# Performance work log

Hardware: AMD Instinct MI355X
Metric: run time of the kernel (lower is better)

## Reference

```python
import jax, jax.numpy as jnp
import numpy as np

OS = 14            # output_size
GRID = 2           # ceil(roi_size/OS) = ceil(28/14) = 2 (boxes are built 28x28, sampling_ratio=-1)
NODES = OS * OS    # 196 graph nodes
EPS = 1e-5         # BatchNorm eps
K, B, C, H, W = 256, 4, 256, 112, 112


def _bn_relu(x, g, b, m, v):
    # eval-mode BatchNorm2d followed by ReLU (bn_act_conv prefix)
    s = jax.lax.rsqrt(v + EPS)
    xn = (x - m[None, :, None, None]) * s[None, :, None, None]
    return jax.nn.relu(xn * g[None, :, None, None] + b[None, :, None, None])


def _conv(x, w, b, pad):
    y = jax.lax.conv_general_dilated(x, w, (1, 1), [(pad, pad), (pad, pad)],
                                     dimension_numbers=('NCHW', 'OIHW', 'NCHW'))
    return y + b[None, :, None, None]


def _roi_align(sem, boxes):
    # torchvision roi_align, spatial_scale=1.0, aligned=False, sampling_ratio=-1 (static grid=2)
    Bs, Cc, Hh, Ww = sem.shape
    bidx = boxes[:, 0].astype(jnp.int32)
    x1, y1, x2, y2 = boxes[:, 1], boxes[:, 2], boxes[:, 3], boxes[:, 4]
    bw = jnp.maximum(x2 - x1, 1.0) / OS
    bh = jnp.maximum(y2 - y1, 1.0) / OS
    t = (jnp.arange(OS * GRID, dtype=sem.dtype) + 0.5) / GRID   # pw*GRID+ix collapsed
    xs = x1[:, None] + bw[:, None] * t                          # [K, 28]
    ys = y1[:, None] + bh[:, None] * t

    def prep(c, L):
        m = (c >= -1.0) & (c <= L)
        cc = jnp.clip(c, 0.0, L - 1)
        lo = jnp.floor(cc).astype(jnp.int32)
        hi = jnp.minimum(lo + 1, L - 1)
        return m, lo, hi, cc - lo

    my, yl, yh, ly = prep(ys, Hh)
    mx, xl, xh, lx = prep(xs, Ww)
    semt = jnp.transpose(sem, (0, 2, 3, 1))  # [B,H,W,C]

    def gat(ya, xa):
        return semt[bidx[:, None, None], ya[:, :, None], xa[:, None, :]]  # [K,28,28,C]

    ly_ = ly[:, :, None, None]
    lx_ = lx[:, None, :, None]
    val = (gat(yl, xl) * (1 - ly_) * (1 - lx_) + gat(yl, xh) * (1 - ly_) * lx_
           + gat(yh, xl) * ly_ * (1 - lx_) + gat(yh, xh) * ly_ * lx_)
    val = jnp.where((my[:, :, None] & mx[:, None, :])[..., None], val, 0.0)
    val = val.reshape(-1, OS, GRID, OS, GRID, Cc).mean(axis=(2, 4))  # avg over sampling grid
    return jnp.transpose(val, (0, 3, 1, 2))  # [K,C,14,14]


def _gcn_agg(A, x):
    # PyG gcn_norm on a fully-connected weighted graph (self loops already present):
    # deg[j] = sum_i A[i,j] (scatter on col); out[j] = sum_i d^-1/2[i] A[i,j] d^-1/2[j] x[i]
    deg = A.sum(axis=1)                 # [K,196]
    dis = jax.lax.rsqrt(deg)            # sigmoid weights > 0 => no zero degree
    Nrm = dis[:, :, None] * A * dis[:, None, :]
    return jnp.einsum('kij,kif->kjf', Nrm, x)


def _forward(roi_feature, semantic, boxes,
             bn_sem_g, bn_sem_b, bn_sem_m, bn_sem_v, conv_sem_w, conv_sem_b,
             bn_fpn_g, bn_fpn_b, bn_fpn_m, bn_fpn_v, conv_fpn_w, conv_fpn_b,
             bn_aff_g, bn_aff_b, bn_aff_m, bn_aff_v, conv_aff_w, conv_aff_b,
             gcn1_w, gcn1_b, gcn2_w, gcn2_b):
    roi_sem = _roi_align(semantic, boxes)                                   # [K,256,14,14]
    a = (_conv(_bn_relu(roi_sem, bn_sem_g, bn_sem_b, bn_sem_m, bn_sem_v), conv_sem_w, conv_sem_b, 1)
         + _conv(_bn_relu(roi_feature, bn_fpn_g, bn_fpn_b, bn_fpn_m, bn_fpn_v), conv_fpn_w, conv_fpn_b, 1))
    aff = _conv(_bn_relu(a, bn_aff_g, bn_aff_b, bn_aff_m, bn_aff_v), conv_aff_w, conv_aff_b, 0)
    A = jax.nn.sigmoid(aff.reshape(-1, NODES, NODES))                       # [K,196,196]
    X = roi_feature.reshape(-1, C, NODES).transpose(0, 2, 1)                # [K,196,256] node feats
    x1 = jax.nn.relu(_gcn_agg(A, X @ gcn1_w) + gcn1_b)                      # GCNConv(256,16)+ReLU
    x2 = _gcn_agg(A, x1 @ gcn2_w) + gcn2_b                                  # GCNConv(16,256)
    emb = x2.transpose(0, 2, 1).reshape(-1, C, OS, OS)
    return roi_sem + emb


def setup_inputs() -> dict:
    key = jax.random.key(0)
    ks = jax.random.split(key, 24)
    roi_feature = jax.random.normal(ks[0], (K, C, OS, OS), jnp.float32)
    semantic = jax.random.normal(ks[1], (B, C, H, W), jnp.float32)
    bidx = jax.random.randint(ks[2], (K,), 0, B).astype(jnp.float32)
    xy = jax.random.uniform(ks[3], (K, 2), jnp.float32, 0.0, float(H - 28))
    boxes = jnp.concatenate([bidx[:, None], xy, xy + 28.0], axis=1)  # (idx,x1,y1,x2,y2), 28x28 boxes

    def bn(kg, c):
        k1, k2, k3, k4 = jax.random.split(kg, 4)
        return (jax.random.normal(k1, (c,)) * 0.1 + 1.0,
                jax.random.normal(k2, (c,)) * 0.1,
                jax.random.normal(k3, (c,)) * 0.1,
                jax.random.uniform(k4, (c,), jnp.float32, 0.5, 1.5))
    bn_sem = bn(ks[4], C); bn_fpn = bn(ks[5], C); bn_aff = bn(ks[6], 64)
    inp = {
        'roi_feature': roi_feature, 'semantic': semantic, 'boxes': boxes,
        'bn_sem_g': bn_sem[0], 'bn_sem_b': bn_sem[1], 'bn_sem_m': bn_sem[2], 'bn_sem_v': bn_sem[3],
        'conv_sem_w': jax.random.normal(ks[7], (64, C, 3, 3)) * 0.02,
        'conv_sem_b': jax.random.normal(ks[8], (64,)) * 0.02,
        'bn_fpn_g': bn_fpn[0], 'bn_fpn_b': bn_fpn[1], 'bn_fpn_m': bn_fpn[2], 'bn_fpn_v': bn_fpn[3],
        'conv_fpn_w': jax.random.normal(ks[9], (64, C, 3, 3)) * 0.02,
        'conv_fpn_b': jax.random.normal(ks[10], (64,)) * 0.02,
        'bn_aff_g': bn_aff[0], 'bn_aff_b': bn_aff[1], 'bn_aff_m': bn_aff[2], 'bn_aff_v': bn_aff[3],
        'conv_aff_w': jax.random.normal(ks[11], (NODES, 64, 1, 1)) * 0.05,
        'conv_aff_b': jax.random.normal(ks[12], (NODES,)) * 0.05,
        'gcn1_w': jax.random.normal(ks[13], (C, 16)) * 0.05,
        'gcn1_b': jax.random.normal(ks[14], (16,)) * 0.05,
        'gcn2_w': jax.random.normal(ks[15], (16, C)) * 0.05,
        'gcn2_b': jax.random.normal(ks[16], (C,)) * 0.05,
    }
    return inp


def reference(roi_feature, semantic, boxes,
              bn_sem_g, bn_sem_b, bn_sem_m, bn_sem_v, conv_sem_w, conv_sem_b,
              bn_fpn_g, bn_fpn_b, bn_fpn_m, bn_fpn_v, conv_fpn_w, conv_fpn_b,
              bn_aff_g, bn_aff_b, bn_aff_m, bn_aff_v, conv_aff_w, conv_aff_b,
              gcn1_w, gcn1_b, gcn2_w, gcn2_b):
    return _forward(roi_feature, semantic, boxes,
                    bn_sem_g, bn_sem_b, bn_sem_m, bn_sem_v, conv_sem_w, conv_sem_b,
                    bn_fpn_g, bn_fpn_b, bn_fpn_m, bn_fpn_v, conv_fpn_w, conv_fpn_b,
                    bn_aff_g, bn_aff_b, bn_aff_m, bn_aff_v, conv_aff_w, conv_aff_b,
                    gcn1_w, gcn1_b, gcn2_w, gcn2_b)
```

## Files before the change

kernel.cpp:

```cpp
#include <hip/hip_runtime.h>
#include <hip/hip_bf16.h>

#define KBOX 256
#define CCH  256
#define NODES 196
#define OS 14

typedef __attribute__((ext_vector_type(8))) short  bf16x8;
typedef __attribute__((ext_vector_type(8))) unsigned short u16x8;
typedef __attribute__((ext_vector_type(4))) float  f32x4;
typedef __attribute__((ext_vector_type(4))) short  s16x4;
typedef __attribute__((ext_vector_type(4))) int    i32x4;

__device__ __forceinline__ short f2bf(float x) {
  __hip_bfloat16 h = __float2bfloat16(x);
  return *reinterpret_cast<short*>(&h);
}
__device__ __forceinline__ float bf2f(unsigned short u) {
  unsigned int x = ((unsigned int)u) << 16;
  union { unsigned int i; float f; } c; c.i = x;
  return c.f;
}

#define MFMA16 __builtin_amdgcn_mfma_f32_16x16x32_bf16

__global__ __launch_bounds__(256) void prep_kernel(
    const float* __restrict__ bn_sem_g, const float* __restrict__ bn_sem_b,
    const float* __restrict__ bn_sem_m, const float* __restrict__ bn_sem_v,
    const float* __restrict__ conv_sem_w, const float* __restrict__ conv_sem_b,
    const float* __restrict__ bn_fpn_g, const float* __restrict__ bn_fpn_b,
    const float* __restrict__ bn_fpn_m, const float* __restrict__ bn_fpn_v,
    const float* __restrict__ conv_fpn_w, const float* __restrict__ conv_fpn_b,
    const float* __restrict__ bn_aff_g, const float* __restrict__ bn_aff_b,
    const float* __restrict__ bn_aff_m, const float* __restrict__ bn_aff_v,
    const float* __restrict__ conv_aff_w, const float* __restrict__ g1w,
    float* __restrict__ ss_sem, float* __restrict__ ss_fpn, float* __restrict__ ss_aff2,
    short* __restrict__ wfrag, short* __restrict__ wafrag, short* __restrict__ g1wf)
{
  int gid = blockIdx.x * blockDim.x + threadIdx.x;
  int gsz = gridDim.x * blockDim.x;
  for (int c = gid; c < 256; c += gsz) {
    float s = bn_sem_g[c] * rsqrtf(bn_sem_v[c] + 1e-5f);
    ss_sem[c] = s; ss_sem[256 + c] = bn_sem_b[c] - bn_sem_m[c] * s;
    float s2 = bn_fpn_g[c] * rsqrtf(bn_fpn_v[c] + 1e-5f);
    ss_fpn[c] = s2; ss_fpn[256 + c] = bn_fpn_b[c] - bn_fpn_m[c] * s2;
  }
  for (int c = gid; c < 64; c += gsz) {
    float s = bn_aff_g[c] * rsqrtf(bn_aff_v[c] + 1e-5f);
    float sh = bn_aff_b[c] - bn_aff_m[c] * s;
    float bias = conv_sem_b[c] + conv_fpn_b[c];
    ss_aff2[c] = s; ss_aff2[64 + c] = bias * s + sh;
  }
  for (int idx = gid; idx < 144 * 4 * 64 * 8; idx += gsz) {
    int e = idx & 7, lane = (idx >> 3) & 63, nt = (idx >> 9) & 3, kstep = idx >> 11;
    int src = kstep / 72, rem = kstep % 72, icc = rem / 9, pos = rem % 9;
    int ky = pos / 3, kx = pos % 3;
    int oc = nt * 16 + (lane & 15);
    int ic = icc * 32 + (lane >> 4) * 8 + e;
    const float* w = src ? conv_fpn_w : conv_sem_w;
    wfrag[idx] = f2bf(w[((oc * 256 + ic) * 3 + ky) * 3 + kx]);
  }
  for (int idx = gid; idx < 2 * 13 * 64 * 8; idx += gsz) {
    int t = idx;
    int e = t & 7; t >>= 3;
    int lane = t & 63; t >>= 6;
    int nt = t % 13; int s = t / 13;
    int i = nt * 16 + (lane & 15);
    int ic = s * 32 + (lane >> 4) * 8 + e;
    wafrag[idx] = f2bf(i < NODES ? conv_aff_w[i * 64 + ic] : 0.f);
  }
  for (int idx = gid; idx < 8 * 64 * 8; idx += gsz) {
    int e = idx & 7, lane = (idx >> 3) & 63, ks = idx >> 9;
    int ic = ks * 32 + (lane >> 4) * 8 + e;
    int f = lane & 15;
    g1wf[idx] = f2bf(g1w[ic * 16 + f]);
  }
}

__global__ __launch_bounds__(256) void transpose_bf16_kernel(
    const float* __restrict__ in, unsigned short* __restrict__ out, int C, int HW)
{
  __shared__ float tile[64][65];
  int nh = (HW + 63) >> 6;
  int bi = blockIdx.x;
  int cb = bi % (C >> 6); bi /= (C >> 6);
  int hb = bi % nh; int b = bi / nh;
  int tx = threadIdx.x & 63, ty = threadIdx.x >> 6;
  const float* inb = in + (size_t)b * C * HW;
  unsigned short* outb = out + (size_t)b * HW * C;
  #pragma unroll
  for (int i = ty; i < 64; i += 4) {
    int c = cb * 64 + i, hw = hb * 64 + tx;
    tile[i][tx] = (hw < HW) ? inb[(size_t)c * HW + hw] : 0.f;
  }
  __syncthreads();
  int cp = threadIdx.x & 31;
  #pragma unroll
  for (int i = (int)(threadIdx.x >> 5); i < 64; i += 8) {
    int hw = hb * 64 + i;
    if (hw < HW) {
      ushort2 v;
      v.x = (unsigned short)f2bf(tile[cp * 2][i]);
      v.y = (unsigned short)f2bf(tile[cp * 2 + 1][i]);
      *(ushort2*)&outb[(size_t)hw * C + cb * 64 + cp * 2] = v;
    }
  }
}

__global__ __launch_bounds__(512) void roi_align_kernel(
    const unsigned short* __restrict__ semt, const float* __restrict__ boxes,
    unsigned short* __restrict__ roi_sem)
{
  __shared__ unsigned short slab[5][29][256];
  int kb = blockIdx.x / 7, g = blockIdx.x % 7;
  int tid = threadIdx.x, wave = tid >> 6, lane = tid & 63;
  const float* bx = boxes + kb * 5;
  int bb = (int)bx[0];
  float x1 = bx[1], y1 = bx[2];
  float xb = x1 + 0.5f, yv = y1 + 0.5f;
  int X0 = (int)floorf(xb); float fx = xb - (float)X0;
  int Y0 = (int)floorf(yv); float fy = yv - (float)Y0;
  const unsigned short* base = semt + (size_t)bb * 12544 * 256;
  #pragma unroll
  for (int i = 0; i < 19; ++i) {
    int s = wave + i * 8;
    if (s < 145) {
      int r = s / 29, xi = s - r * 29;
      int yr = min(Y0 + 4 * g + r, 111);
      int xc = min(X0 + xi, 111);
      *(s16x4*)&slab[r][xi][lane * 4] =
          *(const s16x4*)(base + ((size_t)yr * 112 + xc) * 256 + lane * 4);
    }
  }
  __syncthreads();
  int c2 = tid & 127, grp = tid >> 7;
  int oyl = grp >> 1, og = grp & 1;
  int rb = oyl * 2;
  float w0 = 1.f - fy;
  unsigned short* op = roi_sem + (((size_t)kb * NODES) + (2 * g + oyl) * OS) * 256 + c2 * 2;
  #pragma unroll
  for (int oxs = 0; oxs < 7; ++oxs) {
    int ox = og * 7 + oxs;
    float o0 = 0.f, o1 = 0.f;
    #pragma unroll
    for (int xi = 0; xi < 3; ++xi) {
      float xw = (xi == 0) ? (1.f - fx) : (xi == 1 ? 1.f : fx);
      const unsigned short* p0 = &slab[rb][2 * ox + xi][c2 * 2];
      const unsigned short* p1 = &slab[rb + 1][2 * ox + xi][c2 * 2];
      const unsigned short* p2 = &slab[rb + 2][2 * ox + xi][c2 * 2];
      o0 += xw * (w0 * bf2f(p0[0]) + bf2f(p1[0]) + fy * bf2f(p2[0]));
      o1 += xw * (w0 * bf2f(p0[1]) + bf2f(p1[1]) + fy * bf2f(p2[1]));
    }
    ushort2 v;
    v.x = (unsigned short)f2bf(o0 * 0.25f);
    v.y = (unsigned short)f2bf(o1 * 0.25f);
    *(ushort2*)(op + (size_t)ox * 256) = v;
  }
}

__global__ __launch_bounds__(512) void conv_ab_kernel(
    const unsigned short* __restrict__ roi_sem, const unsigned short* __restrict__ roif,
    const float* __restrict__ ss_sem, const float* __restrict__ ss_fpn,
    const short* __restrict__ wfrag, const float* __restrict__ ss_aff2,
    short* __restrict__ a_rel)
{
  int k = blockIdx.x;
  int tid = threadIdx.x;
  int wave = tid >> 6, lane = tid & 63;
  int l15 = lane & 15, lq = lane >> 4;
  __shared__ short lds_in[197][40];
  __shared__ short lds_wf[18432];
  __shared__ float lds_sc[2][256], lds_sh[2][256];
  __shared__ float scA[64], cmbA[64];

  if (tid < 256) {
    lds_sc[0][tid] = ss_sem[tid]; lds_sh[0][tid] = ss_sem[256 + tid];
    lds_sc[1][tid] = ss_fpn[tid]; lds_sh[1][tid] = ss_fpn[256 + tid];
  }
  if (tid < 64) { scA[tid] = ss_aff2[tid]; cmbA[tid] = ss_aff2[64 + tid]; }
  if (tid < 40) lds_in[196][tid] = 0;

  int mt1 = wave + 8;
  int j0 = wave * 16 + l15;
  int j1 = mt1 * 16 + l15;
  int oy0 = j0 / 14, ox0 = j0 - oy0 * 14;
  int oy1 = j1 / 14, ox1 = j1 - oy1 * 14;
  bool wave_m1 = (mt1 < 13);

  u16x8 inv2[2];
  i32x4 wv[5];
  const size_t kbase = (size_t)k * NODES * CCH;

  f32x4 acc[2][4];
  #pragma unroll
  for (int i = 0; i < 2; ++i)
    #pragma unroll
    for (int j = 0; j < 4; ++j) acc[i][j] = f32x4{0.f, 0.f, 0.f, 0.f};

#define ISSUE_LOADS(P) do {                                                  \
    int src_ = (P) >> 3, icc_ = (P) & 7;                                     \
    const unsigned short* in_ = (src_ ? roif : roi_sem) + kbase + icc_ * 32; \
    inv2[0] = *(const u16x8*)(in_ + (size_t)(tid >> 2) * 256 + (tid & 3) * 8); \
    if (tid < 272) {                                                         \
      int f_ = 512 + tid;                                                    \
      inv2[1] = *(const u16x8*)(in_ + (size_t)(f_ >> 2) * 256 + (f_ & 3) * 8); \
    }                                                                        \
    const i32x4* wsl_ = (const i32x4*)(wfrag + (size_t)(src_ * 72 + icc_ * 9) * 2048); \
    _Pragma("unroll")                                                        \
    for (int i_ = 0; i_ < 4; ++i_) wv[i_] = wsl_[tid + i_ * 512];            \
    if (tid < 256) wv[4] = wsl_[2048 + tid];                                 \
  } while (0)

#define WRITE_STAGE(P) do {                                                  \
    int src_ = (P) >> 3, icc_ = (P) & 7;                                     \
    {                                                                        \
      int j_ = tid >> 2, cq_ = tid & 3;                                      \
      bf16x8 pk_;                                                            \
      _Pragma("unroll")                                                      \
      for (int u_ = 0; u_ < 8; ++u_) {                                       \
        int c_ = icc_ * 32 + cq_ * 8 + u_;                                   \
        float x_ = bf2f(inv2[0][u_]) * lds_sc[src_][c_] + lds_sh[src_][c_];  \
        pk_[u_] = f2bf(fmaxf(x_, 0.f));                                      \
      }                                                                      \
      *(bf16x8*)&lds_in[j_][cq_ * 8] = pk_;                                  \
    }                                                                        \
    if (tid < 272) {                                                         \
      int f_ = 512 + tid; int j_ = f_ >> 2, cq_ = f_ & 3;                    \
      bf16x8 pk_;                                                            \
      _Pragma("unroll")                                                      \
      for (int u_ = 0; u_ < 8; ++u_) {                                       \
        int c_ = icc_ * 32 + cq_ * 8 + u_;                                   \
        float x_ = bf2f(inv2[1][u_]) * lds_sc[src_][c_] + lds_sh[src_][c_];  \
        pk_[u_] = f2bf(fmaxf(x_, 0.f));                                      \
      }                                                                      \
      *(bf16x8*)&lds_in[j_][cq_ * 8] = pk_;                                  \
    }                                                                        \
    _Pragma("unroll")                                                        \
    for (int i_ = 0; i_ < 4; ++i_) ((i32x4*)lds_wf)[tid + i_ * 512] = wv[i_];\
    if (tid < 256) ((i32x4*)lds_wf)[2048 + tid] = wv[4];                     \
  } while (0)

  ISSUE_LOADS(0);
  __syncthreads();
  WRITE_STAGE(0);

  for (int p = 0; p < 16; ++p) {
    __syncthreads();
    if (p < 15) ISSUE_LOADS(p + 1);
    #pragma unroll
    for (int pos = 0; pos < 9; ++pos) {
      int ky = pos / 3 - 1, kx = pos % 3 - 1;
      bf16x8 bfr[4];
      #pragma unroll
      for (int n = 0; n < 4; ++n)
        bfr[n] = *(const bf16x8*)&lds_wf[((pos * 4 + n) * 64 + lane) * 8];
      {
        int ny = oy0 + ky, nx = ox0 + kx;
        bool v = ((unsigned)ny < 14u) & ((unsigned)nx < 14u);
        int np = v ? (ny * 14 + nx) : 196;
        bf16x8 afr = *(const bf16x8*)&lds_in[np][lq * 8];
        acc[0][0] = MFMA16(afr, bfr[0], acc[0][0], 0, 0, 0);
        acc[0][1] = MFMA16(afr, bfr[1], acc[0][1], 0, 0, 0);
        acc[0][2] = MFMA16(afr, bfr[2], acc[0][2], 0, 0, 0);
        acc[0][3] = MFMA16(afr, bfr[3], acc[0][3], 0, 0, 0);
      }
      if (wave_m1) {
        int ny = oy1 + ky, nx = ox1 + kx;
        bool v = (j1 < 196) & ((unsigned)ny < 14u) & ((unsigned)nx < 14u);
        int np = v ? (ny * 14 + nx) : 196;
        bf16x8 afr = *(const bf16x8*)&lds_in[np][lq * 8];
        acc[1][0] = MFMA16(afr, bfr[0], acc[1][0], 0, 0, 0);
        acc[1][1] = MFMA16(afr, bfr[1], acc[1][1], 0, 0, 0);
        acc[1][2] = MFMA16(afr, bfr[2], acc[1][2], 0, 0, 0);
        acc[1][3] = MFMA16(afr, bfr[3], acc[1][3], 0, 0, 0);
      }
    }
    __syncthreads();
    if (p < 15) WRITE_STAGE(p + 1);
  }

  #pragma unroll
  for (int mi = 0; mi < 2; ++mi) {
    int mt = wave + mi * 8;
    if (mt >= 13) continue;
    #pragma unroll
    for (int n = 0; n < 4; ++n) {
      int oc = n * 16 + l15;
      float sa = scA[oc], cb = cmbA[oc];
      #pragma unroll
      for (int r = 0; r < 4; ++r) {
        int j = mt * 16 + lq * 4 + r;
        if (j < NODES) {
          float t = fmaxf(acc[mi][n][r] * sa + cb, 0.f);
          a_rel[((size_t)k * NODES + j) * 64 + oc] = f2bf(t);
        }
      }
    }
  }
#undef ISSUE_LOADS
#undef WRITE_STAGE
}

__global__ __launch_bounds__(512) void graph_kernel(
    const short* __restrict__ a_rel, const short* __restrict__ wafrag,
    const float* __restrict__ aff_b, const short* __restrict__ g1wf,
    const float* __restrict__ g1b, const unsigned short* __restrict__ roif_bf,
    const float* __restrict__ g2w, const float* __restrict__ g2b,
    const unsigned short* __restrict__ roi_sem, float* __restrict__ outp)
{
  __shared__ __align__(16) char smem[160400];
  const int tid = threadIdx.x, wave = tid >> 6, lane = tid & 63;
  const int l15 = lane & 15, lq = lane >> 4;
  const int k = blockIdx.x;

  char*  Ab    = smem;
  char*  U1    = smem + 96512;
  short* lds_a = (short*)(smem + 96512);
  short* wa0   = (short*)(smem + 124736);
  float* zs    = (float*)(smem + 139792);
  short* wa1   = (short*)(smem + 139792);
  short* yfr   = (short*)(smem + 152336);
  float* dsl   = (float*)(smem + 159504);
  float* g1bl  = (float*)(smem + 160336);

  const bool m1 = (wave + 8) < 13;
  const int row0 = wave * 16 + l15;
  const int row1 = (wave + 8) * 16 + l15;
  const int row1c = min(row1, 195);
  i32x4 z4 = {};

  const i32x4* asrc = (const i32x4*)(a_rel + (size_t)k * 12544);
  i32x4 av0 = asrc[tid], av1 = asrc[tid + 512], av2 = asrc[tid + 1024], av3 = z4;
  if (tid < 32) av3 = asrc[1536 + tid];
  const i32x4* wsrc = (const i32x4*)wafrag;
  i32x4 wv0 = wsrc[tid], wv1 = wsrc[tid + 512], wv2 = wsrc[tid + 1024], wv3 = z4;
  if (tid < 128) wv3 = wsrc[1536 + tid];

  for (int idx = tid; idx < 832; idx += 512) {
    int r = idx >> 2, q = idx & 3;
    *(i32x4*)(Ab + r * 464 + 384 + q * 16) = z4;
  }
  if (tid < 16) g1bl[tid] = g1b[tid];

  { int f = tid;        *(i32x4*)(lds_a + (f >> 3) * 72 + (f & 7) * 8) = av0; }
  { int f = tid + 512;  *(i32x4*)(lds_a + (f >> 3) * 72 + (f & 7) * 8) = av1; }
  { int f = tid + 1024; *(i32x4*)(lds_a + (f >> 3) * 72 + (f & 7) * 8) = av2; }
  if (tid < 32) { int f = tid + 1536; *(i32x4*)(lds_a + (f >> 3) * 72 + (f & 7) * 8) = av3; }
  ((i32x4*)wa0)[tid] = wv0;
  if (tid < 320) ((i32x4*)wa0)[512 + tid] = wv1; else ((i32x4*)wa1)[tid - 320] = wv1;
  ((i32x4*)wa1)[192 + tid] = wv2;
  if (tid < 128) ((i32x4*)wa1)[704 + tid] = wv3;
  __syncthreads();

  f32x4 aacc[2][13];
  #pragma unroll
  for (int a = 0; a < 2; ++a)
    #pragma unroll
    for (int b = 0; b < 13; ++b) aacc[a][b] = f32x4{0.f, 0.f, 0.f, 0.f};
  #pragma unroll
  for (int s = 0; s < 2; ++s) {
    const short* was = s ? wa1 : wa0;
    bf16x8 a0 = *(const bf16x8*)(lds_a + row0 * 72 + s * 32 + lq * 8);
    bf16x8 a1 = a0;
    if (m1) a1 = *(const bf16x8*)(lds_a + row1 * 72 + s * 32 + lq * 8);
    #pragma unroll
    for (int n = 0; n < 13; ++n) {
      bf16x8 b = *(const bf16x8*)(was + (n * 64 + lane) * 8);
      aacc[0][n] = MFMA16(a0, b, aacc[0][n], 0, 0, 0);
      if (m1) aacc[1][n] = MFMA16(a1, b, aacc[1][n], 0, 0, 0);
    }
  }
  float rsum0[4] = {0.f, 0.f, 0.f, 0.f}, rsum1[4] = {0.f, 0.f, 0.f, 0.f};
  #pragma unroll
  for (int n = 0; n < 13; ++n) {
    int i = n * 16 + l15;
    bool iv = (i < 196);
    float bv = aff_b[iv ? i : 0];
    #pragma unroll
    for (int r = 0; r < 4; ++r) {
      if (iv) {
        float v0 = aacc[0][n][r] + bv;
        float s0 = 1.f / (1.f + __expf(-v0));
        rsum0[r] += s0;
        *(short*)(Ab + (wave * 16 + lq * 4 + r) * 464 + i * 2) = f2bf(s0);
        if (m1) {
          float v1 = aacc[1][n][r] + bv;
          float s1 = 1.f / (1.f + __expf(-v1));
          rsum1[r] += s1;
          *(short*)(Ab + ((wave + 8) * 16 + lq * 4 + r) * 464 + i * 2) = f2bf(s1);
        }
      }
    }
  }
  #pragma unroll
  for (int r = 0; r < 4; ++r) {
    float v = rsum0[r];
    v += __shfl_xor(v, 1); v += __shfl_xor(v, 2); v += __shfl_xor(v, 4); v += __shfl_xor(v, 8);
    int j = wave * 16 + lq * 4 + r;
    if (l15 == 0) dsl[j] = rsqrtf(v);
    if (m1) {
      float w = rsum1[r];
      w += __shfl_xor(w, 1); w += __shfl_xor(w, 2); w += __shfl_xor(w, 4); w += __shfl_xor(w, 8);
      int j2 = (wave + 8) * 16 + lq * 4 + r;
      if (l15 == 0 && j2 < 196) dsl[j2] = rsqrtf(w);
    }
  }
  __syncthreads();

  float* w2l  = (float*)U1;
  short* g1wl = (short*)(U1 + 17408);
  if (tid < 448) *(i32x4*)((char*)yfr + tid * 16) = z4;
  ((i32x4*)g1wl)[tid] = ((const i32x4*)g1wf)[tid];
  ((f32x4*)w2l)[tid] = ((const f32x4*)g2w)[tid];
  ((f32x4*)w2l)[tid + 512] = ((const f32x4*)g2w)[tid + 512];
  if (tid < 64) ((f32x4*)w2l)[1024 + tid] = ((const f32x4*)g2b)[tid];
  __syncthreads();

  const unsigned short* Xk = roif_bf + (size_t)k * 50176;
  f32x4 xacc0 = f32x4{0.f, 0.f, 0.f, 0.f}, xacc1 = f32x4{0.f, 0.f, 0.f, 0.f};
  #pragma unroll
  for (int ks = 0; ks < 8; ++ks) {
    bf16x8 xb = *(const bf16x8*)(g1wl + (ks * 64 + lane) * 8);
    bf16x8 xa0 = *(const bf16x8*)(Xk + (size_t)row0 * 256 + ks * 32 + lq * 8);
    xacc0 = MFMA16(xa0, xb, xacc0, 0, 0, 0);
    if (m1) {
      bf16x8 xa1 = *(const bf16x8*)(Xk + (size_t)row1c * 256 + ks * 32 + lq * 8);
      xacc1 = MFMA16(xa1, xb, xacc1, 0, 0, 0);
    }
  }

  #pragma unroll
  for (int r = 0; r < 4; ++r) {
    int i = wave * 16 + lq * 4 + r;
    float yv = dsl[i] * xacc0[r];
    yfr[(((i >> 5) * 64) + ((i >> 3) & 3) * 16 + l15) * 8 + (i & 7)] = f2bf(yv);
    if (m1) {
      int i2 = (wave + 8) * 16 + lq * 4 + r;
      if (i2 < 196) {
        float yv2 = dsl[i2] * xacc1[r];
        yfr[(((i2 >> 5) * 64) + ((i2 >> 3) & 3) * 16 + l15) * 8 + (i2 & 7)] = f2bf(yv2);
      }
    }
  }
  __syncthreads();

  f32x4 g0 = f32x4{0.f,0.f,0.f,0.f}, g1v = f32x4{0.f,0.f,0.f,0.f};
  #pragma unroll
  for (int ks = 0; ks < 7; ++ks) {
    bf16x8 bb = *(const bf16x8*)(yfr + (ks * 64 + lane) * 8);
    bf16x8 a0 = *(const bf16x8*)(Ab + row0 * 464 + ks * 64 + lq * 16);
    g0 = MFMA16(a0, bb, g0, 0, 0, 0);
    if (m1) {
      bf16x8 a1 = *(const bf16x8*)(Ab + row1 * 464 + ks * 64 + lq * 16);
      g1v = MFMA16(a1, bb, g1v, 0, 0, 0);
    }
  }
  __syncthreads();
  if (tid < 448) *(i32x4*)((char*)yfr + tid * 16) = z4;
  __syncthreads();
  #pragma unroll
  for (int r = 0; r < 4; ++r) {
    int i = wave * 16 + lq * 4 + r;
    float d = dsl[i];
    float x1v = fmaxf(g0[r] * d + g1bl[l15], 0.f);
    yfr[(((i >> 5) * 64) + ((i >> 3) & 3) * 16 + l15) * 8 + (i & 7)] = f2bf(d * x1v);
    if (m1) {
      int i2 = (wave + 8) * 16 + lq * 4 + r;
      if (i2 < 196) {
        float d2 = dsl[i2];
        float x2v = fmaxf(g1v[r] * d2 + g1bl[l15], 0.f);
        yfr[(((i2 >> 5) * 64) + ((i2 >> 3) & 3) * 16 + l15) * 8 + (i2 & 7)] = f2bf(d2 * x2v);
      }
    }
  }
  __syncthreads();
  f32x4 z0 = f32x4{0.f,0.f,0.f,0.f}, z1v = f32x4{0.f,0.f,0.f,0.f};
  #pragma unroll
  for (int ks = 0; ks < 7; ++ks) {
    bf16x8 bb = *(const bf16x8*)(yfr + (ks * 64 + lane) * 8);
    bf16x8 a0 = *(const bf16x8*)(Ab + row0 * 464 + ks * 64 + lq * 16);
    z0 = MFMA16(a0, bb, z0, 0, 0, 0);
    if (m1) {
      bf16x8 a1 = *(const bf16x8*)(Ab + row1 * 464 + ks * 64 + lq * 16);
      z1v = MFMA16(a1, bb, z1v, 0, 0, 0);
    }
  }
  #pragma unroll
  for (int r = 0; r < 4; ++r) {
    int j = wave * 16 + lq * 4 + r;
    zs[j * 16 + l15] = z0[r] * dsl[j];
    if (m1) {
      int j2 = (wave + 8) * 16 + lq * 4 + r;
      if (j2 < 196) zs[j2 * 16 + l15] = z1v[r] * dsl[j2];
    }
  }
  __syncthreads();

  float* tile = (float*)(U1 + 17408);
  const unsigned short* rsm = roi_sem + (size_t)k * 50176;
  float* op = outp + (size_t)k * 50176;
  for (int cb = 0; cb < 256; cb += 32) {
    #pragma unroll
    for (int rp = 0; rp < 12; ++rp) {
      int e = tid + rp * 512;
      int j = e >> 5, cc = e & 31, c = cb + cc;
      float acc = w2l[4096 + c] + bf2f(rsm[(size_t)j * 256 + c]);
      #pragma unroll
      for (int f = 0; f < 16; ++f) acc += zs[j * 16 + f] * w2l[f * 256 + c];
      tile[j * 33 + cc] = acc;
    }
    if (tid < 128) {
      int e = 6144 + tid;
      int j = e >> 5, cc = e & 31, c = cb + cc;
      float acc = w2l[4096 + c] + bf2f(rsm[(size_t)j * 256 + c]);
      #pragma unroll
      for (int f = 0; f < 16; ++f) acc += zs[j * 16 + f] * w2l[f * 256 + c];
      tile[j * 33 + cc] = acc;
    }
    __syncthreads();
    #pragma unroll
    for (int rp = 0; rp < 12; ++rp) {
      int e = tid + rp * 512;
      int cc = e / 196, j = e - cc * 196;
      op[(size_t)(cb + cc) * 196 + j] = tile[j * 33 + cc];
    }
    if (tid < 128) {
      int e = 6144 + tid;
      int cc = e / 196, j = e - cc * 196;
      op[(size_t)(cb + cc) * 196 + j] = tile[j * 33 + cc];
    }
    __syncthreads();
  }
}

extern "C" void kernel_launch(void* const* d_in, const int* in_sizes, int n_in,
                              void* d_out, int out_size, void* d_ws, size_t ws_size,
                              hipStream_t stream) {
  const float* roi_feature = (const float*)d_in[0];
  const float* semantic    = (const float*)d_in[1];
  const float* boxes       = (const float*)d_in[2];
  const float* bn_sem_g = (const float*)d_in[3];
  const float* bn_sem_b = (const float*)d_in[4];
  const float* bn_sem_m = (const float*)d_in[5];
  const float* bn_sem_v = (const float*)d_in[6];
  const float* conv_sem_w = (const float*)d_in[7];
  const float* conv_sem_b = (const float*)d_in[8];
  const float* bn_fpn_g = (const float*)d_in[9];
  const float* bn_fpn_b = (const float*)d_in[10];
  const float* bn_fpn_m = (const float*)d_in[11];
  const float* bn_fpn_v = (const float*)d_in[12];
  const float* conv_fpn_w = (const float*)d_in[13];
  const float* conv_fpn_b = (const float*)d_in[14];
  const float* bn_aff_g = (const float*)d_in[15];
  const float* bn_aff_b = (const float*)d_in[16];
  const float* bn_aff_m = (const float*)d_in[17];
  const float* bn_aff_v = (const float*)d_in[18];
  const float* conv_aff_w = (const float*)d_in[19];
  const float* conv_aff_b = (const float*)d_in[20];
  const float* gcn1_w = (const float*)d_in[21];
  const float* gcn1_b = (const float*)d_in[22];
  const float* gcn2_w = (const float*)d_in[23];
  const float* gcn2_b = (const float*)d_in[24];

  const size_t FT = (size_t)KBOX * NODES * CCH;
  unsigned short* ws16      = (unsigned short*)d_ws;
  unsigned short* semt_bf   = ws16;
  unsigned short* roif_bf   = semt_bf + FT;
  unsigned short* roi_sem_b = roif_bf + FT;
  short*          a_rel     = (short*)(roi_sem_b + FT);
  float*          ss_sem    = (float*)(a_rel + 3211264);
  float*          ss_fpn    = ss_sem + 512;
  float*          ss_aff2   = ss_fpn + 512;
  short*          wfrag     = (short*)(ss_aff2 + 128);
  short*          wafrag    = wfrag + 294912;
  short*          g1wf      = wafrag + 13312;

  prep_kernel<<<256, 256, 0, stream>>>(
      bn_sem_g, bn_sem_b, bn_sem_m, bn_sem_v, conv_sem_w, conv_sem_b,
      bn_fpn_g, bn_fpn_b, bn_fpn_m, bn_fpn_v, conv_fpn_w, conv_fpn_b,
      bn_aff_g, bn_aff_b, bn_aff_m, bn_aff_v, conv_aff_w, gcn1_w,
      ss_sem, ss_fpn, ss_aff2, wfrag, wafrag, g1wf);

  transpose_bf16_kernel<<<4 * 196 * 4, 256, 0, stream>>>(semantic, semt_bf, 256, 12544);
  transpose_bf16_kernel<<<4 * 4 * 256, 256, 0, stream>>>(roi_feature, roif_bf, 256, 196);
  roi_align_kernel<<<KBOX * 7, 512, 0, stream>>>(semt_bf, boxes, roi_sem_b);
  conv_ab_kernel<<<KBOX, 512, 0, stream>>>(roi_sem_b, roif_bf, ss_sem, ss_fpn, wfrag, ss_aff2, a_rel);
  graph_kernel<<<KBOX, 512, 0, stream>>>(a_rel, wafrag, conv_aff_b, g1wf, gcn1_b, roif_bf,
                                         gcn2_w, gcn2_b, roi_sem_b, (float*)d_out);
}
```

Measured before the change: 160.1 us.

## Restructure graph kernel to 1024 threads and use MFMA for final GCN projection

The graph kernel now runs 16 waves per box, so each of 13 active waves owns one 16-row tile instead of two. It stages the affinity weights in LDS, and replaces the scalar FP32 final projection (z·gcn2_w) with bf16 MFMA using prepacked weight fragments built in the prep kernel. The final output is written directly from MFMA results, with no LDS transpose tile. This is meant to cut scalar FMA work and LDS traffic, at the cost of bf16 rounding in the last matmul and less coalesced strided output stores.

```diff
diff --git a/kernel.cpp b/kernel.cpp
--- a/kernel.cpp
+++ b/kernel.cpp
@@ -34,8 +34,10 @@
     const float* __restrict__ bn_aff_g, const float* __restrict__ bn_aff_b,
     const float* __restrict__ bn_aff_m, const float* __restrict__ bn_aff_v,
     const float* __restrict__ conv_aff_w, const float* __restrict__ g1w,
+    const float* __restrict__ g2w,
     float* __restrict__ ss_sem, float* __restrict__ ss_fpn, float* __restrict__ ss_aff2,
-    short* __restrict__ wfrag, short* __restrict__ wafrag, short* __restrict__ g1wf)
+    short* __restrict__ wfrag, short* __restrict__ wafrag, short* __restrict__ g1wf,
+    short* __restrict__ g2wf)
 {
   int gid = blockIdx.x * blockDim.x + threadIdx.x;
   int gsz = gridDim.x * blockDim.x;
@@ -74,6 +76,12 @@
     int ic = ks * 32 + (lane >> 4) * 8 + e;
     int f = lane & 15;
     g1wf[idx] = f2bf(g1w[ic * 16 + f]);
+  }
+  for (int idx = gid; idx < 16 * 64 * 8; idx += gsz) {
+    int e = idx & 7, lane = (idx >> 3) & 63, ct = idx >> 9;
+    int kk = (lane >> 4) * 8 + e;
+    int c = ct * 16 + (lane & 15);
+    g2wf[idx] = f2bf(kk < 16 ? g2w[kk * 256 + c] : 0.f);
   }
 }
 
@@ -301,235 +309,176 @@
 #undef WRITE_STAGE
 }
 
-__global__ __launch_bounds__(512) void graph_kernel(
+__global__ __launch_bounds__(1024, 1) void graph_kernel(
     const short* __restrict__ a_rel, const short* __restrict__ wafrag,
     const float* __restrict__ aff_b, const short* __restrict__ g1wf,
     const float* __restrict__ g1b, const unsigned short* __restrict__ roif_bf,
-    const float* __restrict__ g2w, const float* __restrict__ g2b,
+    const short* __restrict__ g2wf, const float* __restrict__ g2b,
     const unsigned short* __restrict__ roi_sem, float* __restrict__ outp)
 {
-  __shared__ __align__(16) char smem[160400];
+  __shared__ __align__(16) char smem[125840];
   const int tid = threadIdx.x, wave = tid >> 6, lane = tid & 63;
   const int l15 = lane & 15, lq = lane >> 4;
   const int k = blockIdx.x;
 
-  char*  Ab    = smem;
-  char*  U1    = smem + 96512;
-  short* lds_a = (short*)(smem + 96512);
-  short* wa0   = (short*)(smem + 124736);
-  float* zs    = (float*)(smem + 139792);
-  short* wa1   = (short*)(smem + 139792);
-  short* yfr   = (short*)(smem + 152336);
-  float* dsl   = (float*)(smem + 159504);
-  float* g1bl  = (float*)(smem + 160336);
-
-  const bool m1 = (wave + 8) < 13;
-  const int row0 = wave * 16 + l15;
-  const int row1 = (wave + 8) * 16 + l15;
-  const int row1c = min(row1, 195);
-  i32x4 z4 = {};
-
-  const i32x4* asrc = (const i32x4*)(a_rel + (size_t)k * 12544);
-  i32x4 av0 = asrc[tid], av1 = asrc[tid + 512], av2 = asrc[tid + 1024], av3 = z4;
-  if (tid < 32) av3 = asrc[1536 + tid];
-  const i32x4* wsrc = (const i32x4*)wafrag;
-  i32x4 wv0 = wsrc[tid], wv1 = wsrc[tid + 512], wv2 = wsrc[tid + 1024], wv3 = z4;
-  if (tid < 128) wv3 = wsrc[1536 + tid];
-
-  for (int idx = tid; idx < 832; idx += 512) {
-    int r = idx >> 2, q = idx & 3;
-    *(i32x4*)(Ab + r * 464 + 384 + q * 16) = z4;
-  }
-  if (tid < 16) g1bl[tid] = g1b[tid];
-
-  { int f = tid;        *(i32x4*)(lds_a + (f >> 3) * 72 + (f & 7) * 8) = av0; }
-  { int f = tid + 512;  *(i32x4*)(lds_a + (f >> 3) * 72 + (f & 7) * 8) = av1; }
-  { int f = tid + 1024; *(i32x4*)(lds_a + (f >> 3) * 72 + (f & 7) * 8) = av2; }
-  if (tid < 32) { int f = tid + 1536; *(i32x4*)(lds_a + (f >> 3) * 72 + (f & 7) * 8) = av3; }
-  ((i32x4*)wa0)[tid] = wv0;
-  if (tid < 320) ((i32x4*)wa0)[512 + tid] = wv1; else ((i32x4*)wa1)[tid - 320] = wv1;
-  ((i32x4*)wa1)[192 + tid] = wv2;
-  if (tid < 128) ((i32x4*)wa1)[704 + tid] = wv3;
-  __syncthreads();
-
-  f32x4 aacc[2][13];
-  #pragma unroll
-  for (int a = 0; a < 2; ++a)
-    #pragma unroll
-    for (int b = 0; b < 13; ++b) aacc[a][b] = f32x4{0.f, 0.f, 0.f, 0.f};
-  #pragma unroll
-  for (int s = 0; s < 2; ++s) {
-    const short* was = s ? wa1 : wa0;
-    bf16x8 a0 = *(const bf16x8*)(lds_a + row0 * 72 + s * 32 + lq * 8);
-    bf16x8 a1 = a0;
-    if (m1) a1 = *(const bf16x8*)(lds_a + row1 * 72 + s * 32 + lq * 8);
+  char*  Ab   = smem;
+  short* wa   = (short*)(smem + 96512);
+  short* yfr  = (short*)(smem + 96512);
+  short* zsf  = (short*)(smem + 103680);
+  float* dsl  = (float*)(smem + 123136);
+  float* g1bl = (float*)(smem + 123968);
+  float* g2bl = (float*)(smem + 124032);
+  float* affb = (float*)(smem + 125056);
+
+  const bool wv13 = (wave < 13);
+  const int jr  = wave * 16 + l15;
+  const int jrc = min(jr, 195);
+  const i32x4 z4 = {};
+
+  bf16x8 af0 = {}, af1 = {};
+  if (wv13) {
+    const short* ap = a_rel + (size_t)k * 12544 + jrc * 64 + lq * 8;
+    af0 = *(const bf16x8*)ap;
+    af1 = *(const bf16x8*)(ap + 32);
+  }
+  {
+    i32x4 w0 = ((const i32x4*)wafrag)[tid];
+    i32x4 w1 = z4;
+    if (tid < 640) w1 = ((const i32x4*)wafrag)[1024 + tid];
+    if (tid < 832) {
+      int r = tid >> 2, q = tid & 3;
+      *(i32x4*)(Ab + r * 464 + 384 + q * 16) = z4;
+    }
+    if (tid < 196) affb[tid] = aff_b[tid];
+    if (tid < 256) g2bl[tid] = g2b[tid];
+    if (tid < 16)  g1bl[tid] = g1b[tid];
+    ((i32x4*)wa)[tid] = w0;
+    if (tid < 640) ((i32x4*)wa)[1024 + tid] = w1;
+  }
+  __syncthreads();
+
+  if (wv13) {
+    float rsum[4] = {0.f, 0.f, 0.f, 0.f};
     #pragma unroll
     for (int n = 0; n < 13; ++n) {
-      bf16x8 b = *(const bf16x8*)(was + (n * 64 + lane) * 8);
-      aacc[0][n] = MFMA16(a0, b, aacc[0][n], 0, 0, 0);
-      if (m1) aacc[1][n] = MFMA16(a1, b, aacc[1][n], 0, 0, 0);
-    }
-  }
-  float rsum0[4] = {0.f, 0.f, 0.f, 0.f}, rsum1[4] = {0.f, 0.f, 0.f, 0.f};
-  #pragma unroll
-  for (int n = 0; n < 13; ++n) {
-    int i = n * 16 + l15;
-    bool iv = (i < 196);
-    float bv = aff_b[iv ? i : 0];
+      bf16x8 b0 = *(const bf16x8*)(wa + (n * 64 + lane) * 8);
+      bf16x8 b1 = *(const bf16x8*)(wa + ((13 + n) * 64 + lane) * 8);
+      f32x4 acc = {0.f, 0.f, 0.f, 0.f};
+      acc = MFMA16(af0, b0, acc, 0, 0, 0);
+      acc = MFMA16(af1, b1, acc, 0, 0, 0);
+      int i = n * 16 + l15;
+      bool iv = (i < 196);
+      float bv = affb[iv ? i : 0];
+      #pragma unroll
+      for (int r = 0; r < 4; ++r) {
+        float v = acc[r] + bv;
+        float s = 1.f / (1.f + __expf(-v));
+        if (iv) {
+          rsum[r] += s;
+          *(short*)(Ab + (wave * 16 + lq * 4 + r) * 464 + i * 2) = f2bf(s);
+        }
+      }
+    }
     #pragma unroll
     for (int r = 0; r < 4; ++r) {
-      if (iv) {
-        float v0 = aacc[0][n][r] + bv;
-        float s0 = 1.f / (1.f + __expf(-v0));
-        rsum0[r] += s0;
-        *(short*)(Ab + (wave * 16 + lq * 4 + r) * 464 + i * 2) = f2bf(s0);
-        if (m1) {
-          float v1 = aacc[1][n][r] + bv;
-          float s1 = 1.f / (1.f + __expf(-v1));
-          rsum1[r] += s1;
-          *(short*)(Ab + ((wave + 8) * 16 + lq * 4 + r) * 464 + i * 2) = f2bf(s1);
+      float v = rsum[r];
+      v += __shfl_xor(v, 1); v += __shfl_xor(v, 2);
+      v += __shfl_xor(v, 4); v += __shfl_xor(v, 8);
+      int j = wave * 16 + lq * 4 + r;
+      if (l15 == 0 && j < 196) dsl[j] = rsqrtf(v);
+    }
+  }
+  __syncthreads();
+
+  *(i32x4*)(smem + 96512 + tid * 16) = z4;
+  if (tid < 256) *(i32x4*)(smem + 96512 + (1024 + tid) * 16) = z4;
+  f32x4 xacc = {0.f, 0.f, 0.f, 0.f};
+  if (wv13) {
+    const unsigned short* Xp = roif_bf + (size_t)k * 50176 + (size_t)jrc * 256 + lq * 8;
+    #pragma unroll
+    for (int ks = 0; ks < 8; ++ks) {
+      bf16x8 xa = *(const bf16x8*)(Xp + ks * 32);
+      bf16x8 xb = *(const bf16x8*)(g1wf + (ks * 64 + lane) * 8);
+      xacc = MFMA16(xa, xb, xacc, 0, 0, 0);
+    }
+  }
+  __syncthreads();
+
+  if (wv13) {
+    #pragma unroll
+    for (int r = 0; r < 4; ++r) {
+      int i = wave * 16 + lq * 4 + r;
+      if (i < 196) {
+        float yv = dsl[i] * xacc[r];
+        yfr[((i >> 5) * 64 + ((i >> 3) & 3) * 16 + l15) * 8 + (i & 7)] = f2bf(yv);
+      }
+    }
+  }
+  __syncthreads();
+
+  f32x4 g0 = {0.f, 0.f, 0.f, 0.f};
+  if (wv13) {
+    #pragma unroll
+    for (int ks = 0; ks < 7; ++ks) {
+      bf16x8 bb = *(const bf16x8*)(yfr + (ks * 64 + lane) * 8);
+      bf16x8 a0 = *(const bf16x8*)(Ab + jr * 464 + ks * 64 + lq * 16);
+      g0 = MFMA16(a0, bb, g0, 0, 0, 0);
+    }
+  }
+  __syncthreads();
+  if (wv13) {
+    #pragma unroll
+    for (int r = 0; r < 4; ++r) {
+      int i = wave * 16 + lq * 4 + r;
+      if (i < 196) {
+        float d = dsl[i];
+        float x1v = fmaxf(g0[r] * d + g1bl[l15], 0.f);
+        yfr[((i >> 5) * 64 + ((i >> 3) & 3) * 16 + l15) * 8 + (i & 7)] = f2bf(d * x1v);
+      }
+    }
+  }
+  __syncthreads();
+
+  if (wv13) {
+    f32x4 z0 = {0.f, 0.f, 0.f, 0.f};
+    #pragma unroll
+    for (int ks = 0; ks < 7; ++ks) {
+      bf16x8 bb = *(const bf16x8*)(yfr + (ks * 64 + lane) * 8);
+      bf16x8 a0 = *(const bf16x8*)(Ab + jr * 464 + ks * 64 + lq * 16);
+      z0 = MFMA16(a0, bb, z0, 0, 0, 0);
+    }
+    #pragma unroll
+    for (int r = 0; r < 4; ++r) {
+      int j = wave * 16 + lq * 4 + r;
+      if (j < 196) {
+        float zv = z0[r] * dsl[j];
+        zsf[((j >> 4) * 64 + (l15 >> 3) * 16 + (j & 15)) * 8 + (l15 & 7)] = f2bf(zv);
+      }
+    }
+  }
+  __syncthreads();
+
+  {
+    bf16x8 wf = *(const bf16x8*)(g2wf + (wave * 64 + lane) * 8);
+    const unsigned short* rsmk = roi_sem + (size_t)k * 50176;
+    float* op = outp + (size_t)k * 50176;
+    float gbv[4];
+    #pragma unroll
+    for (int r = 0; r < 4; ++r) gbv[r] = g2bl[wave * 16 + lq * 4 + r];
+    #pragma unroll
+    for (int jt = 0; jt < 13; ++jt) {
+      bf16x8 zb = *(const bf16x8*)(zsf + (jt * 64 + lane) * 8);
+      f32x4 d = {0.f, 0.f, 0.f, 0.f};
+      d = MFMA16(wf, zb, d, 0, 0, 0);
+      int j = jt * 16 + l15;
+      if (j < 196) {
+        #pragma unroll
+        for (int r = 0; r < 4; ++r) {
+          int c = wave * 16 + lq * 4 + r;
+          op[(size_t)c * 196 + j] = d[r] + gbv[r] + bf2f(rsmk[(size_t)j * 256 + c]);
         }
       }
     }
-  }
-  #pragma unroll
-  for (int r = 0; r < 4; ++r) {
-    float v = rsum0[r];
-    v += __shfl_xor(v, 1); v += __shfl_xor(v, 2); v += __shfl_xor(v, 4); v += __shfl_xor(v, 8);
-    int j = wave * 16 + lq * 4 + r;
-    if (l15 == 0) dsl[j] = rsqrtf(v);
-    if (m1) {
-      float w = rsum1[r];
-      w += __shfl_xor(w, 1); w += __shfl_xor(w, 2); w += __shfl_xor(w, 4); w += __shfl_xor(w, 8);
-      int j2 = (wave + 8) * 16 + lq * 4 + r;
-      if (l15 == 0 && j2 < 196) dsl[j2] = rsqrtf(w);
-    }
-  }
-  __syncthreads();
-
-  float* w2l  = (float*)U1;
-  short* g1wl = (short*)(U1 + 17408);
-  if (tid < 448) *(i32x4*)((char*)yfr + tid * 16) = z4;
-  ((i32x4*)g1wl)[tid] = ((const i32x4*)g1wf)[tid];
-  ((f32x4*)w2l)[tid] = ((const f32x4*)g2w)[tid];
-  ((f32x4*)w2l)[tid + 512] = ((const f32x4*)g2w)[tid + 512];
-  if (tid < 64) ((f32x4*)w2l)[1024 + tid] = ((const f32x4*)g2b)[tid];
-  __syncthreads();
-
-  const unsigned short* Xk = roif_bf + (size_t)k * 50176;
-  f32x4 xacc0 = f32x4{0.f, 0.f, 0.f, 0.f}, xacc1 = f32x4{0.f, 0.f, 0.f, 0.f};
-  #pragma unroll
-  for (int ks = 0; ks < 8; ++ks) {
-    bf16x8 xb = *(const bf16x8*)(g1wl + (ks * 64 + lane) * 8);
-    bf16x8 xa0 = *(const bf16x8*)(Xk + (size_t)row0 * 256 + ks * 32 + lq * 8);
-    xacc0 = MFMA16(xa0, xb, xacc0, 0, 0, 0);
-    if (m1) {
-      bf16x8 xa1 = *(const bf16x8*)(Xk + (size_t)row1c * 256 + ks * 32 + lq * 8);
-      xacc1 = MFMA16(xa1, xb, xacc1, 0, 0, 0);
-    }
-  }
-
-  #pragma unroll
-  for (int r = 0; r < 4; ++r) {
-    int i = wave * 16 + lq * 4 + r;
-    float yv = dsl[i] * xacc0[r];
-    yfr[(((i >> 5) * 64) + ((i >> 3) & 3) * 16 + l15) * 8 + (i & 7)] = f2bf(yv);
-    if (m1) {
-      int i2 = (wave + 8) * 16 + lq * 4 + r;
-      if (i2 < 196) {
-        float yv2 = dsl[i2] * xacc1[r];
-        yfr[(((i2 >> 5) * 64) + ((i2 >> 3) & 3) * 16 + l15) * 8 + (i2 & 7)] = f2bf(yv2);
-      }
-    }
-  }
-  __syncthreads();
-
-  f32x4 g0 = f32x4{0.f,0.f,0.f,0.f}, g1v = f32x4{0.f,0.f,0.f,0.f};
-  #pragma unroll
-  for (int ks = 0; ks < 7; ++ks) {
-    bf16x8 bb = *(const bf16x8*)(yfr + (ks * 64 + lane) * 8);
-    bf16x8 a0 = *(const bf16x8*)(Ab + row0 * 464 + ks * 64 + lq * 16);
-    g0 = MFMA16(a0, bb, g0, 0, 0, 0);
-    if (m1) {
-      bf16x8 a1 = *(const bf16x8*)(Ab + row1 * 464 + ks * 64 + lq * 16);
-      g1v = MFMA16(a1, bb, g1v, 0, 0, 0);
-    }
-  }
-  __syncthreads();
-  if (tid < 448) *(i32x4*)((char*)yfr + tid * 16) = z4;
-  __syncthreads();
-  #pragma unroll
-  for (int r = 0; r < 4; ++r) {
-    int i = wave * 16 + lq * 4 + r;
-    float d = dsl[i];
-    float x1v = fmaxf(g0[r] * d + g1bl[l15], 0.f);
-    yfr[(((i >> 5) * 64) + ((i >> 3) & 3) * 16 + l15) * 8 + (i & 7)] = f2bf(d * x1v);
-    if (m1) {
-      int i2 = (wave + 8) * 16 + lq * 4 + r;
-      if (i2 < 196) {
-        float d2 = dsl[i2];
-        float x2v = fmaxf(g1v[r] * d2 + g1bl[l15], 0.f);
-        yfr[(((i2 >> 5) * 64) + ((i2 >> 3) & 3) * 16 + l15) * 8 + (i2 & 7)] = f2bf(d2 * x2v);
-      }
-    }
-  }
-  __syncthreads();
-  f32x4 z0 = f32x4{0.f,0.f,0.f,0.f}, z1v = f32x4{0.f,0.f,0.f,0.f};
-  #pragma unroll
-  for (int ks = 0; ks < 7; ++ks) {
-    bf16x8 bb = *(const bf16x8*)(yfr + (ks * 64 + lane) * 8);
-    bf16x8 a0 = *(const bf16x8*)(Ab + row0 * 464 + ks * 64 + lq * 16);
-    z0 = MFMA16(a0, bb, z0, 0, 0, 0);
-    if (m1) {
-      bf16x8 a1 = *(const bf16x8*)(Ab + row1 * 464 + ks * 64 + lq * 16);
-      z1v = MFMA16(a1, bb, z1v, 0, 0, 0);
-    }
-  }
-  #pragma unroll
-  for (int r = 0; r < 4; ++r) {
-    int j = wave * 16 + lq * 4 + r;
-    zs[j * 16 + l15] = z0[r] * dsl[j];
-    if (m1) {
-      int j2 = (wave + 8) * 16 + lq * 4 + r;
-      if (j2 < 196) zs[j2 * 16 + l15] = z1v[r] * dsl[j2];
-    }
-  }
-  __syncthreads();
-
-  float* tile = (float*)(U1 + 17408);
-  const unsigned short* rsm = roi_sem + (size_t)k * 50176;
-  float* op = outp + (size_t)k * 50176;
-  for (int cb = 0; cb < 256; cb += 32) {
-    #pragma unroll
-    for (int rp = 0; rp < 12; ++rp) {
-      int e = tid + rp * 512;
-      int j = e >> 5, cc = e & 31, c = cb + cc;
-      float acc = w2l[4096 + c] + bf2f(rsm[(size_t)j * 256 + c]);
-      #pragma unroll
-      for (int f = 0; f < 16; ++f) acc += zs[j * 16 + f] * w2l[f * 256 + c];
-      tile[j * 33 + cc] = acc;
-    }
-    if (tid < 128) {
-      int e = 6144 + tid;
-      int j = e >> 5, cc = e & 31, c = cb + cc;
-      float acc = w2l[4096 + c] + bf2f(rsm[(size_t)j * 256 + c]);
-      #pragma unroll
-      for (int f = 0; f < 16; ++f) acc += zs[j * 16 + f] * w2l[f * 256 + c];
-      tile[j * 33 + cc] = acc;
-    }
-    __syncthreads();
-    #pragma unroll
-    for (int rp = 0; rp < 12; ++rp) {
-      int e = tid + rp * 512;
-      int cc = e / 196, j = e - cc * 196;
-      op[(size_t)(cb + cc) * 196 + j] = tile[j * 33 + cc];
-    }
-    if (tid < 128) {
-      int e = 6144 + tid;
-      int cc = e / 196, j = e - cc * 196;
-      op[(size_t)(cb + cc) * 196 + j] = tile[j * 33 + cc];
-    }
-    __syncthreads();
   }
 }
 
@@ -574,17 +523,18 @@
   short*          wfrag     = (short*)(ss_aff2 + 128);
   short*          wafrag    = wfrag + 294912;
   short*          g1wf      = wafrag + 13312;
+  short*          g2wf      = g1wf + 4096;
 
   prep_kernel<<<256, 256, 0, stream>>>(
       bn_sem_g, bn_sem_b, bn_sem_m, bn_sem_v, conv_sem_w, conv_sem_b,
       bn_fpn_g, bn_fpn_b, bn_fpn_m, bn_fpn_v, conv_fpn_w, conv_fpn_b,
-      bn_aff_g, bn_aff_b, bn_aff_m, bn_aff_v, conv_aff_w, gcn1_w,
-      ss_sem, ss_fpn, ss_aff2, wfrag, wafrag, g1wf);
+      bn_aff_g, bn_aff_b, bn_aff_m, bn_aff_v, conv_aff_w, gcn1_w, gcn2_w,
+      ss_sem, ss_fpn, ss_aff2, wfrag, wafrag, g1wf, g2wf);
 
   transpose_bf16_kernel<<<4 * 196 * 4, 256, 0, stream>>>(semantic, semt_bf, 256, 12544);
   transpose_bf16_kernel<<<4 * 4 * 256, 256, 0, stream>>>(roi_feature, roif_bf, 256, 196);
   roi_align_kernel<<<KBOX * 7, 512, 0, stream>>>(semt_bf, boxes, roi_sem_b);
   conv_ab_kernel<<<KBOX, 512, 0, stream>>>(roi_sem_b, roif_bf, ss_sem, ss_fpn, wfrag, ss_aff2, a_rel);
-  graph_kernel<<<KBOX, 512, 0, stream>>>(a_rel, wafrag, conv_aff_b, g1wf, gcn1_b, roif_bf,
-                                         gcn2_w, gcn2_b, roi_sem_b, (float*)d_out);
-}
+  graph_kernel<<<KBOX, 1024, 0, stream>>>(a_rel, wafrag, conv_aff_b, g1wf, gcn1_b, roif_bf,
+                                          g2wf, gcn2_b, roi_sem_b, (float*)d_out);
+}
```

Result: faster. 142.3 us (-11.1%).
